# Optimization experiments

Measured on AMD Instinct MI355X. Metric: run time of the kernel, lower is better.

Reference implementation:

```python
import jax, jax.numpy as jnp
import numpy as np
import math

B, N, D = 32, 1024, 512
S, R = 4, 64  # num_space, in_channels // reduction
EPS = 1e-12
COUNT = B  # self.count += b on first call
SCALE = 1.718 * math.exp(-COUNT / 30000.0) - 0.718


def sparsemax(z, axis=-1):
    # Martins & Astudillo sparsemax along `axis` (size K)
    K = z.shape[axis]
    z_sorted = -jnp.sort(-z, axis=axis)  # descending
    k = jnp.arange(1, K + 1, dtype=z.dtype).reshape((1,) * (z.ndim - 1) + (K,))
    k = jnp.moveaxis(k, -1, axis)
    z_cumsum = jnp.cumsum(z_sorted, axis=axis)
    support = (k * z_sorted > z_cumsum - 1).astype(z.dtype)
    k_sup = jnp.sum(support, axis=axis, keepdims=True)
    idx = (k_sup - 1).astype(jnp.int32)
    tau = (jnp.take_along_axis(z_cumsum, idx, axis=axis) - 1) / k_sup
    return jnp.maximum(z - tau, 0.0)


def setup_inputs() -> dict:
    key = jax.random.key(0)
    k1, k2, k3 = jax.random.split(key, 3)
    x = jax.random.normal(k1, (B, N, D), dtype=jnp.float32)
    mask = jax.random.randint(k2, (B,), 1, N + 1)  # valid token counts, >=1
    subspace = jax.random.normal(k3, (S, R, D), dtype=jnp.float32)
    return {"x": x, "mask": mask, "subspace": subspace}


def reference(x, mask, subspace):
    b, n, d = x.shape
    # BaseAggregator: L2-normalize tokens (F.normalize, p=2, dim=2)
    xn = x / jnp.maximum(jnp.linalg.norm(x, axis=2, keepdims=True), EPS)
    # project_matrix = subspace^T @ subspace / (d * scale); apply in two low-rank
    # steps to avoid per-token dxd matvec: y = S x, proj = S^T y
    y = jnp.einsum('skd,bnd->bnsk', subspace, xn)          # [b,n,S,R]
    proj = jnp.einsum('skd,bnsk->bnsd', subspace, y)       # [b,n,S,D]
    proj = proj / (d * SCALE)
    projection = jnp.linalg.norm(proj, axis=3)             # [b,n,S]
    probability = sparsemax(projection, axis=2)            # [b,n,S]
    max_indices = jnp.argmax(probability, axis=2)          # [b,n]
    # majority vote over valid tokens (bincount+argmax, vectorized)
    valid = (jnp.arange(n)[None, :] < mask[:, None])       # [b,n]
    onehot = jax.nn.one_hot(max_indices, S, dtype=jnp.float32) * valid[..., None]
    counts = onehot.sum(axis=1)                            # [b,S]
    vote = jnp.argmax(counts, axis=1)                      # [b]
    weights = jnp.take_along_axis(probability, vote[:, None, None], axis=2)[..., 0]  # [b,n]
    feature = jnp.sum(xn * weights[:, :, None], axis=1)    # [b,d]
    return feature
```

## Files before the change

### kernel.cpp

```cpp
#include <hip/hip_runtime.h>
#include <math.h>

#define BB 32
#define NN 1024
#define DD 512
#define SS 4
#define RR 64
#define OUTC 256
#define NT (BB*NN)
#define MT 64
#define NBLK (NT/MT)
#define BPB (NN/MT)

typedef float4 f4;
typedef float f32x4 __attribute__((ext_vector_type(4)));
typedef __bf16 bf16x8 __attribute__((ext_vector_type(8)));
typedef unsigned short u16x8 __attribute__((ext_vector_type(8)));
typedef const __attribute__((address_space(1))) void GVoid;
typedef __attribute__((address_space(3))) void LVoid;

union BF8 { u16x8 u; bf16x8 b; unsigned w[4]; };

__device__ __forceinline__ float hif(float f) {
  return __uint_as_float(__float_as_uint(f) & 0xffff0000u);
}
__device__ __forceinline__ unsigned short topu(float f) {
  return (unsigned short)(__float_as_uint(f) >> 16);
}
__device__ __forceinline__ unsigned pack2(float e0, float e1) {
  return __builtin_amdgcn_perm(__float_as_uint(e1), __float_as_uint(e0), 0x07060302u);
}

#define MFMA(a,b,c) __builtin_amdgcn_mfma_f32_16x16x32_bf16((a),(b),(c),0,0,0)

#define BARRIER_LGKM() do { \
  asm volatile("s_waitcnt lgkmcnt(0)" ::: "memory"); \
  __builtin_amdgcn_s_barrier(); \
} while (0)
#define WAITV(N) asm volatile("s_waitcnt vmcnt(" #N ")" ::: "memory")

__global__ __launch_bounds__(256) void prep_kernel(const float* __restrict__ sub,
    unsigned short* __restrict__ subhi, unsigned short* __restrict__ sublo,
    unsigned short* __restrict__ Ghi, unsigned short* __restrict__ Glo) {
  int t = threadIdx.x, blk = blockIdx.x;
  __shared__ __align__(16) float Sl[64][36];
  if (blk < 128) {
    int i = (blk*256 + t)*4;
    f4 v = *(const f4*)&sub[i];
    uint2 hh, ll;
    hh.x = pack2(v.x, v.y); hh.y = pack2(v.z, v.w);
    ll.x = pack2(v.x - hif(v.x), v.y - hif(v.y));
    ll.y = pack2(v.z - hif(v.z), v.w - hif(v.w));
    *(uint2*)&subhi[i] = hh;
    *(uint2*)&sublo[i] = ll;
    return;
  }
  int s = blk - 128;
  int lane = t & 63, w = t >> 6, l15 = lane & 15, l4 = lane >> 4;
  int row = t >> 2, seg = t & 3;
  f4 r0, r1;
  f32x4 acc[4] = {{0,0,0,0},{0,0,0,0},{0,0,0,0},{0,0,0,0}};
  {
    const float* p = &sub[(size_t)(s*RR + row)*DD + seg*8];
    r0 = *(const f4*)p; r1 = *(const f4*)(p+4);
  }
  for (int kc = 0; kc < 16; ++kc) {
    __syncthreads();
    *(f4*)&Sl[row][seg*8]   = r0;
    *(f4*)&Sl[row][seg*8+4] = r1;
    __syncthreads();
    if (kc < 15) {
      const float* p = &sub[(size_t)(s*RR + row)*DD + (kc+1)*32 + seg*8];
      r0 = *(const f4*)p; r1 = *(const f4*)(p+4);
    }
    BF8 ah, al;
    {
      int ra = w*16 + l15;
      f32x4 v0 = *(const f32x4*)&Sl[ra][l4*8];
      f32x4 v1 = *(const f32x4*)&Sl[ra][l4*8+4];
      float ff[8] = {v0[0],v0[1],v0[2],v0[3],v1[0],v1[1],v1[2],v1[3]};
#pragma unroll
      for (int e = 0; e < 8; ++e) { ah.u[e] = topu(ff[e]); al.u[e] = topu(ff[e]-hif(ff[e])); }
    }
#pragma unroll
    for (int j = 0; j < 4; ++j) {
      BF8 bh, bl;
      int rb = j*16 + l15;
      f32x4 v0 = *(const f32x4*)&Sl[rb][l4*8];
      f32x4 v1 = *(const f32x4*)&Sl[rb][l4*8+4];
      float ff[8] = {v0[0],v0[1],v0[2],v0[3],v1[0],v1[1],v1[2],v1[3]};
#pragma unroll
      for (int e = 0; e < 8; ++e) { bh.u[e] = topu(ff[e]); bl.u[e] = topu(ff[e]-hif(ff[e])); }
      acc[j] = MFMA(ah.b, bh.b, acc[j]);
      acc[j] = MFMA(ah.b, bl.b, acc[j]);
      acc[j] = MFMA(al.b, bh.b, acc[j]);
    }
  }
#pragma unroll
  for (int j = 0; j < 4; ++j)
#pragma unroll
    for (int r = 0; r < 4; ++r) {
      int grow = w*16 + l4*4 + r, gcol = j*16 + l15;
      float v = acc[j][r];
      Ghi[((size_t)s*RR + grow)*RR + gcol] = topu(v);
      Glo[((size_t)s*RR + grow)*RR + gcol] = topu(v - hif(v));
    }
}

__global__ __launch_bounds__(512, 4) void fused_kernel(
    const float* __restrict__ x,
    const unsigned short* __restrict__ subhi, const unsigned short* __restrict__ sublo,
    const unsigned short* __restrict__ Ghi, const unsigned short* __restrict__ Glo,
    float inv_denom, int* __restrict__ amax, float* __restrict__ partial) {
  __shared__ __align__(16) float stage4[4][2048];
  __shared__ float ssqlds[64];
  __shared__ float prq2[64][4][2];
  __shared__ float Wl[64][4];

  int t = threadIdx.x;
  int lane = t & 63, w = t >> 6;
  int s = w & 3, ch = w >> 2;
  int l15 = lane & 15, l4 = lane >> 4;
  int m0 = blockIdx.x * MT;

  f32x4 acc[4][2] = {};
  float ssq4[4] = {0.f, 0.f, 0.f, 0.f};

  int drow = t >> 3, dsp = t & 7;
  const float* dsrc0 = &x[(size_t)(m0 + drow)*DD + (dsp ^ (drow & 7))*4];
  auto stage = [&](int p) {
    __builtin_amdgcn_global_load_lds((GVoid*)(dsrc0 + p*32),
        (LVoid*)((char*)&stage4[p & 3][0] + t*16), 16, 0, 0);
  };
  auto loadB = [&](BF8 (&bh)[2], BF8 (&bl)[2], int kc) {
#pragma unroll
    for (int nf = 0; nf < 2; ++nf) {
      size_t off = (size_t)(s*64 + ch*32 + nf*16 + l15)*DD + kc*32 + l4*8;
      bh[nf].u = *(const u16x8*)&subhi[off];
      bl[nf].u = *(const u16x8*)&sublo[off];
    }
  };
  auto kstep = [&](int p, BF8 (&bh)[2], BF8 (&bl)[2]) {
    const char* base = (const char*)&stage4[p & 3][0];
#pragma unroll
    for (int mf = 0; mf < 4; ++mf) {
      int row = mf*16 + l15;
      int ph0 = (2*l4) ^ (row & 7), ph1 = (2*l4 + 1) ^ (row & 7);
      f32x4 v0 = *(const f32x4*)(base + row*128 + ph0*16);
      f32x4 v1 = *(const f32x4*)(base + row*128 + ph1*16);
      float f0=v0[0], f1=v0[1], f2=v0[2], f3=v0[3];
      float g4=v1[0], g5=v1[1], g6=v1[2], g7=v1[3];
      if (w == 0)
        ssq4[mf] += f0*f0+f1*f1+f2*f2+f3*f3+g4*g4+g5*g5+g6*g6+g7*g7;
      BF8 ah, al;
      ah.w[0] = pack2(f0,f1); ah.w[1] = pack2(f2,f3);
      ah.w[2] = pack2(g4,g5); ah.w[3] = pack2(g6,g7);
      al.w[0] = pack2(f0-hif(f0), f1-hif(f1));
      al.w[1] = pack2(f2-hif(f2), f3-hif(f3));
      al.w[2] = pack2(g4-hif(g4), g5-hif(g5));
      al.w[3] = pack2(g6-hif(g6), g7-hif(g7));
#pragma unroll
      for (int nf = 0; nf < 2; ++nf) {
        acc[mf][nf] = MFMA(ah.b, bh[nf].b, acc[mf][nf]);
        acc[mf][nf] = MFMA(ah.b, bl[nf].b, acc[mf][nf]);
        acc[mf][nf] = MFMA(al.b, bh[nf].b, acc[mf][nf]);
      }
    }
  };

  BF8 bh[2], bl[2];
  loadB(bh, bl, 0);
  stage(0); stage(1); stage(2);
  WAITV(2);
#pragma unroll
  for (int p = 0; p < 16; ++p) {
    BARRIER_LGKM();
    if (p + 3 < 16) stage(p + 3);
    kstep(p, bh, bl);
    if (p + 1 < 16) loadB(bh, bl, p + 1);
    if      (p == 0)  WAITV(7);
    else if (p == 1)  WAITV(10);
    else if (p <= 12) WAITV(14);
    else if (p == 13) WAITV(13);
    else if (p == 14) WAITV(12);
  }

  if (w == 0) {
#pragma unroll
    for (int mf = 0; mf < 4; ++mf) {
      float v = ssq4[mf];
      v += __shfl_xor(v, 16); v += __shfl_xor(v, 32);
      if (lane < 16) ssqlds[mf*16 + lane] = v;
    }
  }

  BF8 gh[2][2], gl2[2][2];
#pragma unroll
  for (int kf = 0; kf < 2; ++kf)
#pragma unroll
    for (int nf = 0; nf < 2; ++nf) {
      size_t off = (size_t)(s*RR + (ch*2 + nf)*16 + l15)*RR + kf*32 + l4*8;
      gh[kf][nf].u  = *(const u16x8*)&Ghi[off];
      gl2[kf][nf].u = *(const u16x8*)&Glo[off];
    }
  __syncthreads();

  float* ysc = &stage4[0][0];
#pragma unroll
  for (int h = 0; h < 4; ++h) {
#pragma unroll
    for (int nf = 0; nf < 2; ++nf)
#pragma unroll
      for (int r = 0; r < 4; ++r)
        ysc[s*1088 + (l4*4 + r)*68 + ch*32 + nf*16 + l15] = acc[h][nf][r];
    __syncthreads();
    BF8 yh[2], yl[2];
#pragma unroll
    for (int kf = 0; kf < 2; ++kf) {
      int base = s*1088 + l15*68 + kf*32 + l4*8;
      f32x4 v0 = *(const f32x4*)&ysc[base];
      f32x4 v1 = *(const f32x4*)&ysc[base+4];
      float ff[8] = {v0[0],v0[1],v0[2],v0[3],v1[0],v1[1],v1[2],v1[3]};
#pragma unroll
      for (int e = 0; e < 8; ++e) {
        yh[kf].u[e] = topu(ff[e]);
        yl[kf].u[e] = topu(ff[e] - hif(ff[e]));
      }
    }
    f32x4 z[2] = {};
#pragma unroll
    for (int nf = 0; nf < 2; ++nf)
#pragma unroll
      for (int kf = 0; kf < 2; ++kf) {
        z[nf] = MFMA(yh[kf].b, gh[kf][nf].b,  z[nf]);
        z[nf] = MFMA(yh[kf].b, gl2[kf][nf].b, z[nf]);
        z[nf] = MFMA(yl[kf].b, gh[kf][nf].b,  z[nf]);
      }
#pragma unroll
    for (int r = 0; r < 4; ++r) {
      float qp = z[0][r]*acc[h][0][r] + z[1][r]*acc[h][1][r];
      qp += __shfl_xor(qp, 1); qp += __shfl_xor(qp, 2);
      qp += __shfl_xor(qp, 4); qp += __shfl_xor(qp, 8);
      if (l15 == 0) prq2[h*16 + l4*4 + r][s][ch] = qp;
    }
    __syncthreads();
  }

  if (t < MT) {
    float ss = ssqlds[t];
    float inv = 1.f / fmaxf(sqrtf(ss), 1e-12f);
    float p0 = sqrtf(fmaxf(prq2[t][0][0] + prq2[t][0][1], 0.f)) * inv * inv_denom;
    float p1 = sqrtf(fmaxf(prq2[t][1][0] + prq2[t][1][1], 0.f)) * inv * inv_denom;
    float p2 = sqrtf(fmaxf(prq2[t][2][0] + prq2[t][2][1], 0.f)) * inv * inv_denom;
    float p3 = sqrtf(fmaxf(prq2[t][3][0] + prq2[t][3][1], 0.f)) * inv * inv_denom;
    float a0=p0, a1=p1, a2=p2, a3=p3, hi, lo;
    hi = fmaxf(a0,a1); lo = fminf(a0,a1); a0=hi; a1=lo;
    hi = fmaxf(a2,a3); lo = fminf(a2,a3); a2=hi; a3=lo;
    hi = fmaxf(a0,a2); lo = fminf(a0,a2); a0=hi; a2=lo;
    hi = fmaxf(a1,a3); lo = fminf(a1,a3); a1=hi; a3=lo;
    hi = fmaxf(a1,a2); lo = fminf(a1,a2); a1=hi; a2=lo;
    float c2 = a0+a1, c3 = c2+a2, c4s = c3+a3;
    int ksup = 1 + (2.f*a1 > c2-1.f) + (3.f*a2 > c3-1.f) + (4.f*a3 > c4s-1.f);
    float csel = (ksup==1) ? a0 : (ksup==2) ? c2 : (ksup==3) ? c3 : c4s;
    float tau = (csel - 1.f) / (float)ksup;
    float q0 = fmaxf(p0-tau, 0.f), q1 = fmaxf(p1-tau, 0.f);
    float q2 = fmaxf(p2-tau, 0.f), q3 = fmaxf(p3-tau, 0.f);
    int arg = 0; float best = q0;
    if (q1 > best) { best = q1; arg = 1; }
    if (q2 > best) { best = q2; arg = 2; }
    if (q3 > best) { best = q3; arg = 3; }
    amax[m0 + t] = arg;
    Wl[t][0] = q0*inv; Wl[t][1] = q1*inv; Wl[t][2] = q2*inv; Wl[t][3] = q3*inv;
  }
  __syncthreads();

  {
    int grp = t >> 7, dcol = t & 127;
    f32x4 a0 = {0,0,0,0};
#pragma unroll 8
    for (int tok = 0; tok < MT; ++tok) {
      f32x4 v = *(const f32x4*)&x[(size_t)(m0 + tok)*DD + dcol*4];
      a0 += v * Wl[tok][grp];
    }
    *(f32x4*)&partial[((size_t)blockIdx.x*4 + grp)*DD + dcol*4] = a0;
  }
}

__global__ __launch_bounds__(256) void finish_kernel(const int* __restrict__ amax,
    const float* __restrict__ partial, const int* __restrict__ mask,
    float* __restrict__ out) {
  __shared__ int cnt[4];
  __shared__ int vsh;
  int bb = blockIdx.x, t = threadIdx.x;
  if (t < 4) cnt[t] = 0;
  __syncthreads();
  int m = mask[bb];
  int c0=0, c1=0, c2=0, c3=0;
  for (int n = t; n < NN; n += 256) {
    if (n < m) {
      int a = amax[bb*NN + n];
      c0 += (a==0); c1 += (a==1); c2 += (a==2); c3 += (a==3);
    }
  }
  atomicAdd(&cnt[0], c0); atomicAdd(&cnt[1], c1);
  atomicAdd(&cnt[2], c2); atomicAdd(&cnt[3], c3);
  __syncthreads();
  if (t == 0) {
    int arg = 0, best = cnt[0];
    if (cnt[1] > best) { best = cnt[1]; arg = 1; }
    if (cnt[2] > best) { best = cnt[2]; arg = 2; }
    if (cnt[3] > best) { best = cnt[3]; arg = 3; }
    vsh = arg;
  }
  __syncthreads();
  int v = vsh;
  for (int d = t; d < DD; d += 256) {
    float f = 0.f;
#pragma unroll
    for (int c = 0; c < BPB; ++c)
      f += partial[(((size_t)(bb*BPB + c))*4 + v)*DD + d];
    out[bb*DD + d] = f;
  }
}

extern "C" void kernel_launch(void* const* d_in, const int* in_sizes, int n_in,
                              void* d_out, int out_size, void* d_ws, size_t ws_size,
                              hipStream_t stream) {
  const float* x    = (const float*)d_in[0];
  const int*   mask = (const int*)d_in[1];
  const float* sub  = (const float*)d_in[2];
  float* out = (float*)d_out;

  float* partial = (float*)d_ws;
  int*   amax    = (int*)(partial + (size_t)NBLK*4*DD);
  unsigned short* subhi = (unsigned short*)(amax + NT);
  unsigned short* sublo = subhi + OUTC*DD;
  unsigned short* Ghi   = sublo + OUTC*DD;
  unsigned short* Glo   = Ghi + SS*RR*RR;

  double scale = 1.718 * exp(-((double)BB) / 30000.0) - 0.718;
  float inv_denom = (float)(1.0 / ((double)DD * scale));

  prep_kernel<<<128 + SS, 256, 0, stream>>>(sub, subhi, sublo, Ghi, Glo);
  fused_kernel<<<NBLK, 512, 0, stream>>>(x, subhi, sublo, Ghi, Glo, inv_denom, amax, partial);
  finish_kernel<<<BB, 256, 0, stream>>>(amax, partial, mask, out);
}
```

Before: 76.19 us.

## Load activations directly into registers instead of async LDS staging; split finish kernel

The fused kernel stops staging x tiles through LDS with async global_load_lds, manual vmcnt waits and per-step barriers. Each lane now loads its A fragments straight from global memory into registers, double-buffering the B fragments and interleaving the next chunk's loads with the MFMAs. This removes the barriers and LDS traffic from the main loop, but raises register pressure and gives up the shared cooperative loads. The finish kernel also launches eight blocks per batch, each reducing a 64-column slice, to get more parallelism; the vote counting is now repeated in every block.

```diff
diff --git a/kernel.cpp b/kernel.cpp
--- a/kernel.cpp
+++ b/kernel.cpp
@@ -16,8 +16,6 @@
 typedef float f32x4 __attribute__((ext_vector_type(4)));
 typedef __bf16 bf16x8 __attribute__((ext_vector_type(8)));
 typedef unsigned short u16x8 __attribute__((ext_vector_type(8)));
-typedef const __attribute__((address_space(1))) void GVoid;
-typedef __attribute__((address_space(3))) void LVoid;
 
 union BF8 { u16x8 u; bf16x8 b; unsigned w[4]; };
 
@@ -32,12 +30,6 @@
 }
 
 #define MFMA(a,b,c) __builtin_amdgcn_mfma_f32_16x16x32_bf16((a),(b),(c),0,0,0)
-
-#define BARRIER_LGKM() do { \
-  asm volatile("s_waitcnt lgkmcnt(0)" ::: "memory"); \
-  __builtin_amdgcn_s_barrier(); \
-} while (0)
-#define WAITV(N) asm volatile("s_waitcnt vmcnt(" #N ")" ::: "memory")
 
 __global__ __launch_bounds__(256) void prep_kernel(const float* __restrict__ sub,
     unsigned short* __restrict__ subhi, unsigned short* __restrict__ sublo,
@@ -112,7 +104,7 @@
     const unsigned short* __restrict__ subhi, const unsigned short* __restrict__ sublo,
     const unsigned short* __restrict__ Ghi, const unsigned short* __restrict__ Glo,
     float inv_denom, int* __restrict__ amax, float* __restrict__ partial) {
-  __shared__ __align__(16) float stage4[4][2048];
+  __shared__ __align__(16) float ysc[4*1088];
   __shared__ float ssqlds[64];
   __shared__ float prq2[64][4][2];
   __shared__ float Wl[64][4];
@@ -123,31 +115,49 @@
   int l15 = lane & 15, l4 = lane >> 4;
   int m0 = blockIdx.x * MT;
 
+  const float* aBase = &x[(size_t)(m0 + l15)*DD + l4*8];
+  const unsigned short* bhBase = &subhi[(size_t)(s*64 + ch*32 + l15)*DD + l4*8];
+  const unsigned short* blBase = &sublo[(size_t)(s*64 + ch*32 + l15)*DD + l4*8];
+
   f32x4 acc[4][2] = {};
   float ssq4[4] = {0.f, 0.f, 0.f, 0.f};
 
-  int drow = t >> 3, dsp = t & 7;
-  const float* dsrc0 = &x[(size_t)(m0 + drow)*DD + (dsp ^ (drow & 7))*4];
-  auto stage = [&](int p) {
-    __builtin_amdgcn_global_load_lds((GVoid*)(dsrc0 + p*32),
-        (LVoid*)((char*)&stage4[p & 3][0] + t*16), 16, 0, 0);
+  f32x4 rawA[4][2];
+  BF8 Bh[2][2], Bl[2][2];
+
+  auto loadA01 = [&](int c) {
+#pragma unroll
+    for (int mf = 0; mf < 2; ++mf) {
+      const float* p = aBase + (size_t)(mf*16)*DD + c*32;
+      rawA[mf][0] = *(const f32x4*)p;
+      rawA[mf][1] = *(const f32x4*)(p + 4);
+    }
   };
-  auto loadB = [&](BF8 (&bh)[2], BF8 (&bl)[2], int kc) {
+  auto loadA23 = [&](int c) {
+#pragma unroll
+    for (int mf = 2; mf < 4; ++mf) {
+      const float* p = aBase + (size_t)(mf*16)*DD + c*32;
+      rawA[mf][0] = *(const f32x4*)p;
+      rawA[mf][1] = *(const f32x4*)(p + 4);
+    }
+  };
+  auto loadB = [&](int buf, int c) {
 #pragma unroll
     for (int nf = 0; nf < 2; ++nf) {
-      size_t off = (size_t)(s*64 + ch*32 + nf*16 + l15)*DD + kc*32 + l4*8;
-      bh[nf].u = *(const u16x8*)&subhi[off];
-      bl[nf].u = *(const u16x8*)&sublo[off];
+      size_t off = (size_t)(nf*16)*DD + c*32;
+      Bh[buf][nf].u = *(const u16x8*)(bhBase + off);
+      Bl[buf][nf].u = *(const u16x8*)(blBase + off);
     }
   };
-  auto kstep = [&](int p, BF8 (&bh)[2], BF8 (&bl)[2]) {
-    const char* base = (const char*)&stage4[p & 3][0];
+
+  loadA01(0); loadA23(0);
+  loadB(0, 0);
+#pragma unroll
+  for (int c = 0; c < 16; ++c) {
+    const int cur = c & 1, nxt = cur ^ 1;
 #pragma unroll
     for (int mf = 0; mf < 4; ++mf) {
-      int row = mf*16 + l15;
-      int ph0 = (2*l4) ^ (row & 7), ph1 = (2*l4 + 1) ^ (row & 7);
-      f32x4 v0 = *(const f32x4*)(base + row*128 + ph0*16);
-      f32x4 v1 = *(const f32x4*)(base + row*128 + ph1*16);
+      f32x4 v0 = rawA[mf][0], v1 = rawA[mf][1];
       float f0=v0[0], f1=v0[1], f2=v0[2], f3=v0[3];
       float g4=v1[0], g5=v1[1], g6=v1[2], g7=v1[3];
       if (w == 0)
@@ -161,28 +171,13 @@
       al.w[3] = pack2(g6-hif(g6), g7-hif(g7));
 #pragma unroll
       for (int nf = 0; nf < 2; ++nf) {
-        acc[mf][nf] = MFMA(ah.b, bh[nf].b, acc[mf][nf]);
-        acc[mf][nf] = MFMA(ah.b, bl[nf].b, acc[mf][nf]);
-        acc[mf][nf] = MFMA(al.b, bh[nf].b, acc[mf][nf]);
+        acc[mf][nf] = MFMA(ah.b, Bh[cur][nf].b, acc[mf][nf]);
+        acc[mf][nf] = MFMA(ah.b, Bl[cur][nf].b, acc[mf][nf]);
+        acc[mf][nf] = MFMA(al.b, Bh[cur][nf].b, acc[mf][nf]);
       }
-    }
-  };
-
-  BF8 bh[2], bl[2];
-  loadB(bh, bl, 0);
-  stage(0); stage(1); stage(2);
-  WAITV(2);
-#pragma unroll
-  for (int p = 0; p < 16; ++p) {
-    BARRIER_LGKM();
-    if (p + 3 < 16) stage(p + 3);
-    kstep(p, bh, bl);
-    if (p + 1 < 16) loadB(bh, bl, p + 1);
-    if      (p == 0)  WAITV(7);
-    else if (p == 1)  WAITV(10);
-    else if (p <= 12) WAITV(14);
-    else if (p == 13) WAITV(13);
-    else if (p == 14) WAITV(12);
+      if (mf == 1 && c < 15) loadA01(c + 1);
+      if (mf == 3 && c < 15) { loadA23(c + 1); loadB(nxt, c + 1); }
+    }
   }
 
   if (w == 0) {
@@ -203,9 +198,7 @@
       gh[kf][nf].u  = *(const u16x8*)&Ghi[off];
       gl2[kf][nf].u = *(const u16x8*)&Glo[off];
     }
-  __syncthreads();
-
-  float* ysc = &stage4[0][0];
+
 #pragma unroll
   for (int h = 0; h < 4; ++h) {
 #pragma unroll
@@ -291,7 +284,8 @@
     float* __restrict__ out) {
   __shared__ int cnt[4];
   __shared__ int vsh;
-  int bb = blockIdx.x, t = threadIdx.x;
+  int bb = blockIdx.x >> 3, slice = blockIdx.x & 7;
+  int t = threadIdx.x;
   if (t < 4) cnt[t] = 0;
   __syncthreads();
   int m = mask[bb];
@@ -314,7 +308,8 @@
   }
   __syncthreads();
   int v = vsh;
-  for (int d = t; d < DD; d += 256) {
+  if (t < 64) {
+    int d = slice*64 + t;
     float f = 0.f;
 #pragma unroll
     for (int c = 0; c < BPB; ++c)
@@ -343,5 +338,5 @@
 
   prep_kernel<<<128 + SS, 256, 0, stream>>>(sub, subhi, sublo, Ghi, Glo);
   fused_kernel<<<NBLK, 512, 0, stream>>>(x, subhi, sublo, Ghi, Glo, inv_denom, amax, partial);
-  finish_kernel<<<BB, 256, 0, stream>>>(amax, partial, mask, out);
-}
+  finish_kernel<<<BB*8, 256, 0, stream>>>(amax, partial, mask, out);
+}
```

New measurement: 129.5 us. +70.0%, slower.
